# Optimization experiments

Hardware: AMD Instinct MI355X
Metric: run time of the kernel (lower is better)

## Reference

```python
import jax, jax.numpy as jnp
import numpy as np

B, L, K, D = 1, 4096, 24, 512


def setup_inputs() -> dict:
    key = jax.random.key(0)
    k1, k2, k3, k4 = jax.random.split(key, 4)
    u = jax.random.normal(k1, (B, L, D), dtype=jnp.float32)
    # spectral filter bank (learned parameter initialized from Hankel eigenvectors in the
    # original; random init is equivalent for a correctness baseline), scaled ~O(1/sqrt(L))
    filters = jax.random.normal(k2, (L, K), dtype=jnp.float32) * (1.0 / np.sqrt(L))
    M_phi_plus = jax.random.normal(k3, (K, D, D), dtype=jnp.float32) * (1.0 / np.sqrt(K * D))
    M_phi_minus = jax.random.normal(k4, (K, D, D), dtype=jnp.float32) * (1.0 / np.sqrt(K * D))
    return {"u": u, "filters": filters, "M_phi_plus": M_phi_plus, "M_phi_minus": M_phi_minus}


def _causal_conv(u, phi):
    # Causal linear convolution of every input channel with every spectral filter via FFT.
    # u: [B, L, D], phi: [L, K] -> [B, L, K, D]
    L_ = u.shape[1]
    n = 2 * L_  # zero-pad so circular FFT conv == linear causal conv
    Uf = jnp.fft.rfft(u, n=n, axis=1)                    # [B, F, D]
    Pf = jnp.fft.rfft(phi, n=n, axis=0)                  # [F, K]
    prod = Uf[:, :, None, :] * Pf[None, :, :, None]      # [B, F, K, D]
    return jnp.fft.irfft(prod, n=n, axis=1)[:, :L_]      # [B, L, K, D]


def reference(u, filters, M_phi_plus, M_phi_minus):
    L_ = u.shape[1]
    # sgn[t] = (-1)^t ; U_minus[b,l,k,d] = sum_s u[b,s,d] * phi[l-s,k] * (-1)^(l-s),
    # which equals convolving with the alternating-sign filter phi[t]*(-1)^t
    # (the original implements this as sgn-pre/post-multiplication around FlashFFTConv).
    sgn = jnp.where(jnp.arange(L_) % 2 == 0, 1.0, -1.0).astype(u.dtype)
    U_plus = _causal_conv(u, filters)                      # [B, L, K, D]
    U_minus = _causal_conv(u, filters * sgn[:, None])      # [B, L, K, D]
    y = (jnp.einsum('blkd,kdo->blo', U_plus, M_phi_plus)
         + jnp.einsum('blkd,kdo->blo', U_minus, M_phi_minus))
    return y
```

## Files before the change

### kernel.cpp

```cpp
#include <hip/hip_runtime.h>
#include <hip/hip_bf16.h>
#include <cstdint>
#include <cstddef>

using bf16 = __hip_bfloat16;

typedef __attribute__((ext_vector_type(4))) float f32x4;
typedef __attribute__((ext_vector_type(8))) short s16x8;

#define LSEQ 4096
#define DDIM 512
#define KFLT 24
#define NFFT 8192
#define FPAD 4224
#define MROWS 8448
#define FLIVE 8194

__device__ __forceinline__ void gld16(const bf16* g, bf16* l) {
  __builtin_amdgcn_global_load_lds((const __attribute__((address_space(1))) void*)g,
                                   (__attribute__((address_space(3))) void*)l, 16, 0, 0);
}

#define MEMFENCE asm volatile("" ::: "memory")
#define BAR() do { MEMFENCE; __builtin_amdgcn_s_barrier(); MEMFENCE; } while (0)

__device__ __forceinline__ float fsin_rev(float rev) {
  float s; asm("v_sin_f32 %0, %1" : "=v"(s) : "v"(rev)); return s;
}
__device__ __forceinline__ float fcos_rev(float rev) {
  float c; asm("v_cos_f32 %0, %1" : "=v"(c) : "v"(rev)); return c;
}

__device__ __forceinline__ void stage_half(const bf16* g, int ldk, bf16* ldsbase,
                                           int wave, int lane) {
  const int r8 = lane >> 3;
  const int sc = ((lane & 7) ^ r8) * 8;
  #pragma unroll
  for (int q = 0; q < 2; ++q) {
    const int c = wave * 2 + q;
    gld16(g + (size_t)(c * 8 + r8) * ldk + sc, ldsbase + c * 512);
  }
}

__device__ __forceinline__ s16x8 ldfrag(const bf16* buf, int row, int kk, int l4) {
  return *(const s16x8*)(buf + row * 64 + (((kk * 4 + l4) ^ (row & 7)) * 8));
}

__global__ __launch_bounds__(256) void transpose_cast(
    const float* __restrict__ in, bf16* __restrict__ out, int R, int C) {
  __shared__ float tile[32][33];
  const size_t bo = (size_t)blockIdx.z * R * C;
  const float* inb = in + bo;
  bf16* outb = out + bo;
  int c0 = blockIdx.x * 32, r0 = blockIdx.y * 32;
  int tx = threadIdx.x & 31, ty = threadIdx.x >> 5;
  #pragma unroll
  for (int i = 0; i < 32; i += 8)
    tile[ty + i][tx] = inb[(size_t)(r0 + ty + i) * C + (c0 + tx)];
  __syncthreads();
  #pragma unroll
  for (int i = 0; i < 32; i += 8)
    outb[(size_t)(c0 + ty + i) * R + (r0 + tx)] = __float2bfloat16(tile[tx][ty + i]);
}

__global__ __launch_bounds__(256) void tr_reduce5(
    const float* __restrict__ P0, const float* __restrict__ P14,
    bf16* __restrict__ out) {
  __shared__ float tile[32][33];
  int c0 = blockIdx.x * 32, r0 = blockIdx.y * 32;
  int tx = threadIdx.x & 31, ty = threadIdx.x >> 5;
  const size_t MN = (size_t)MROWS * DDIM;
  #pragma unroll
  for (int i = 0; i < 32; i += 8) {
    size_t idx = (size_t)(r0 + ty + i) * DDIM + (c0 + tx);
    tile[ty + i][tx] = P0[idx] + P14[idx] + P14[idx + MN] +
                       P14[idx + 2 * MN] + P14[idx + 3 * MN];
  }
  __syncthreads();
  #pragma unroll
  for (int i = 0; i < 32; i += 8)
    out[(size_t)(c0 + ty + i) * MROWS + (r0 + tx)] = __float2bfloat16(tile[tx][ty + i]);
}

__global__ __launch_bounds__(256) void reduce4(
    const float* __restrict__ P, float* __restrict__ y) {
  size_t i = ((size_t)blockIdx.x * 256 + threadIdx.x) * 4;
  const size_t MN = (size_t)LSEQ * DDIM;
  f32x4 a = *(const f32x4*)(P + i);
  f32x4 b = *(const f32x4*)(P + i + MN);
  f32x4 c = *(const f32x4*)(P + i + 2 * MN);
  f32x4 d = *(const f32x4*)(P + i + 3 * MN);
  *(f32x4*)(y + i) = a + b + c + d;
}

__global__ __launch_bounds__(256) void gen_w(bf16* __restrict__ W) {
  int r = blockIdx.y;
  int t0 = (blockIdx.x * 256 + threadIdx.x) * 8;
  bf16 o[8];
  if (r < FLIVE) {
    int f = r >> 1;
    bool odd = r & 1;
    #pragma unroll
    for (int i = 0; i < 8; ++i) {
      int m = (f * (t0 + i)) & (NFFT - 1);
      float rev = (float)m * (1.f / NFFT);
      float v = odd ? -fsin_rev(rev) : fcos_rev(rev);
      o[i] = __float2bfloat16(v);
    }
  } else {
    #pragma unroll
    for (int i = 0; i < 8; ++i) o[i] = __float2bfloat16(0.f);
  }
  *(s16x8*)(W + (size_t)r * LSEQ + t0) = *(const s16x8*)o;
}

__global__ __launch_bounds__(256) void gen_cinv(bf16* __restrict__ Cinv) {
  int l = blockIdx.y;
  int r0 = (blockIdx.x * 256 + threadIdx.x) * 8;
  if (r0 >= MROWS) return;
  bf16 o[8];
  #pragma unroll
  for (int p = 0; p < 4; ++p) {
    int rr = r0 + 2 * p;
    float v0 = 0.f, v1 = 0.f;
    if (rr < FLIVE) {
      int f = rr >> 1;
      int m = (f * l) & (NFFT - 1);
      float rev = (float)m * (1.f / NFFT);
      float wf = (f == 0 || f == NFFT / 2) ? 1.f : 2.f;
      float sc = wf * (1.f / NFFT);
      v0 = sc * fcos_rev(rev);
      v1 = -sc * fsin_rev(rev);
    }
    o[2 * p] = __float2bfloat16(v0);
    o[2 * p + 1] = __float2bfloat16(v1);
  }
  *(s16x8*)(Cinv + (size_t)l * MROWS + r0) = *(const s16x8*)o;
}

__global__ __launch_bounds__(256) void compute_pf(
    const float* __restrict__ phi, float* __restrict__ Pf) {
  int f = blockIdx.x;
  int tid = threadIdx.x;
  int lane = tid & 63, wave = tid >> 6;
  float pre[KFLT], pim[KFLT];
  #pragma unroll
  for (int k = 0; k < KFLT; ++k) { pre[k] = 0.f; pim[k] = 0.f; }
  for (int cch = 0; cch < LSEQ / 256; ++cch) {
    int t = cch * 256 + tid;
    int m = (f * t) & (NFFT - 1);
    float rev = (float)m * (1.f / NFFT);
    float s = fsin_rev(rev), c = fcos_rev(rev);
    const float4* pv = (const float4*)(phi + (size_t)t * KFLT);
    float4 v0 = pv[0], v1 = pv[1], v2 = pv[2], v3 = pv[3], v4 = pv[4], v5 = pv[5];
    float pr[KFLT] = {v0.x, v0.y, v0.z, v0.w, v1.x, v1.y, v1.z, v1.w,
                      v2.x, v2.y, v2.z, v2.w, v3.x, v3.y, v3.z, v3.w,
                      v4.x, v4.y, v4.z, v4.w, v5.x, v5.y, v5.z, v5.w};
    #pragma unroll
    for (int k = 0; k < KFLT; ++k) {
      pre[k] += pr[k] * c;
      pim[k] -= pr[k] * s;
    }
  }
  __shared__ float red[4][2 * KFLT];
  #pragma unroll
  for (int k = 0; k < KFLT; ++k) {
    float r = pre[k], i2 = pim[k];
    #pragma unroll
    for (int off = 32; off > 0; off >>= 1) {
      r += __shfl_down(r, off, 64);
      i2 += __shfl_down(i2, off, 64);
    }
    if (lane == 0) { red[wave][2 * k] = r; red[wave][2 * k + 1] = i2; }
  }
  __syncthreads();
  if (tid < 2 * KFLT)
    Pf[(size_t)f * (2 * KFLT) + tid] =
        red[0][tid] + red[1][tid] + red[2][tid] + red[3][tid];
}

__global__ __launch_bounds__(256) void build_pw(
    const float* __restrict__ Pf, float* __restrict__ Pw) {
  int idx = blockIdx.x * 256 + threadIdx.x;
  if (idx >= 48 * FPAD) return;
  int j = idx / FPAD, f = idx % FPAD;
  float re = 0.f, im = 0.f;
  if (f <= NFFT / 2) {
    if (j < KFLT) {
      re = Pf[(size_t)f * 48 + j * 2];
      im = Pf[(size_t)f * 48 + j * 2 + 1];
    } else {
      int k = j - KFLT, g = NFFT / 2 - f;
      re = Pf[(size_t)g * 48 + k * 2];
      im = -Pf[(size_t)g * 48 + k * 2 + 1];
    }
  }
  Pw[(size_t)idx * 2] = re;
  Pw[(size_t)idx * 2 + 1] = im;
}

template <int STORE>
__global__ __launch_bounds__(512, 2) void gemmD(
    const bf16* __restrict__ A, const bf16* __restrict__ Bt, int ldk,
    bf16* __restrict__ Obf, float* __restrict__ Of) {
  __shared__ bf16 sA[2 * 128 * 64];
  __shared__ bf16 sB[2 * 256 * 64];

  const int nwg = gridDim.x;
  const int lin = blockIdx.x;
  const int q8 = nwg >> 3, r8g = nwg & 7;
  const int xcd = lin & 7, pos = lin >> 3;
  const int wid = (xcd < r8g ? xcd * (q8 + 1) : r8g * (q8 + 1) + (xcd - r8g) * q8) + pos;

  int by, bx, kt0, nkt, ks;
  if constexpr (STORE == 0) { by = wid % 66; bx = wid / 66; kt0 = 0; nkt = 64; ks = 0; }
  else { int xy = wid & 63; ks = wid >> 6; by = xy >> 1; bx = xy & 1; kt0 = ks * 33; nkt = 33; }

  const int tid = threadIdx.x, lane = tid & 63, wave = tid >> 6;
  const int l15 = lane & 15, l4 = lane >> 4;
  const int wr = wave >> 2, wc = wave & 3;
  const int mtile = by * 128, ntile = bx * 256;
  const bf16* Ab = A + (size_t)mtile * ldk;
  const bf16* Bb = Bt + (size_t)ntile * ldk;

  f32x4 acc[4][4];
  #pragma unroll
  for (int m = 0; m < 4; ++m)
    #pragma unroll
    for (int n = 0; n < 4; ++n) acc[m][n] = f32x4{0.f, 0.f, 0.f, 0.f};

  stage_half(Ab + (size_t)kt0 * 64, ldk, sA, wave, lane);
  stage_half(Bb + (size_t)kt0 * 64, ldk, sB, wave, lane);
  stage_half(Bb + (size_t)128 * ldk + (size_t)kt0 * 64, ldk, sB + 128 * 64, wave, lane);
  asm volatile("s_waitcnt vmcnt(0)" ::: "memory");
  BAR();

  for (int t = 0; t < nkt; ++t) {
    const int par = t & 1, nb = par ^ 1;
    const bf16* bA = sA + par * (128 * 64);
    const bf16* bB = sB + par * (256 * 64);
    const bool more = (t + 1 < nkt);

    s16x8 afr[4][2], bfr[4][2];
    #pragma unroll
    for (int n = 0; n < 4; ++n)
      #pragma unroll
      for (int kk = 0; kk < 2; ++kk)
        bfr[n][kk] = ldfrag(bB, wc * 64 + n * 16 + l15, kk, l4);
    #pragma unroll
    for (int m = 0; m < 4; ++m)
      #pragma unroll
      for (int kk = 0; kk < 2; ++kk)
        afr[m][kk] = ldfrag(bA, wr * 64 + m * 16 + l15, kk, l4);

    if (more) {
      const size_t ko = (size_t)(kt0 + t + 1) * 64;
      stage_half(Ab + ko, ldk, sA + nb * (128 * 64), wave, lane);
      stage_half(Bb + ko, ldk, sB + nb * (256 * 64), wave, lane);
      stage_half(Bb + (size_t)128 * ldk + ko, ldk, sB + nb * (256 * 64) + 128 * 64,
                 wave, lane);
    }

    __builtin_amdgcn_s_setprio(1);
    #pragma unroll
    for (int m = 0; m < 4; ++m)
      #pragma unroll
      for (int n = 0; n < 4; ++n)
        #pragma unroll
        for (int kk = 0; kk < 2; ++kk)
          acc[m][n] = __builtin_amdgcn_mfma_f32_16x16x32_bf16(
              afr[m][kk], bfr[n][kk], acc[m][n], 0, 0, 0);
    __builtin_amdgcn_s_setprio(0);

    asm volatile("s_waitcnt vmcnt(0)" ::: "memory");
    BAR();
  }

  #pragma unroll
  for (int m = 0; m < 4; ++m)
    #pragma unroll
    for (int n = 0; n < 4; ++n)
      #pragma unroll
      for (int e = 0; e < 4; ++e) {
        int row = mtile + wr * 64 + m * 16 + l4 * 4 + e;
        int col = ntile + wc * 64 + n * 16 + l15;
        if constexpr (STORE == 0)
          Obf[(size_t)row * DDIM + col] = __float2bfloat16(acc[m][n][e]);
        else
          Of[(size_t)ks * LSEQ * DDIM + (size_t)row * DDIM + col] = acc[m][n][e];
      }
}

__global__ __launch_bounds__(512, 2) void gemmW(
    const bf16* __restrict__ Auf, const bf16* __restrict__ Mt,
    const float* __restrict__ Pw, float* __restrict__ P0, float* __restrict__ P14) {
  __shared__ bf16 sA[2 * 256 * 64];
  __shared__ bf16 sB[2 * 256 * 64];

  const int lin = blockIdx.x;
  const int wid = (lin & 7) * 32 + (lin >> 3);
  const int tid = threadIdx.x, lane = tid & 63, wave = tid >> 6;
  const int l15 = lane & 15, l4 = lane >> 4;
  const int wr = wave >> 2, wc = wave & 3;
  const int r8 = lane >> 3, c8 = lane & 7;
  const float sgn = (r8 & 1) ? 1.f : -1.f;

  const int g0 = wid * 99, g1 = g0 + 99;

  float* dst = (wid % 5 == 0) ? P0
             : P14 + (size_t)(wid % 5 - 1) * ((size_t)MROWS * DDIM);

  f32x4 acc[8][4];
  #pragma unroll
  for (int m = 0; m < 8; ++m)
    #pragma unroll
    for (int n = 0; n < 4; ++n) acc[m][n] = f32x4{0.f, 0.f, 0.f, 0.f};

  int4 adat[4];
  float2 wv[4];

  auto decode = [&](int g, int& mt, int& nt, int& j, int& kt, int& xy) {
    xy = g / 384; int rem = g - xy * 384; j = rem >> 3; kt = rem & 7;
    mt = (xy % 33) * 256; nt = (xy / 33) * 256;
  };
  auto issueA = [&](int mt, int j, int kt) {
    #pragma unroll
    for (int q = 0; q < 4; ++q) {
      int rl = (q >> 1) * 128 + (wave * 2 + (q & 1)) * 8 + r8;
      int rowg = mt + rl;
      adat[q] = *(const int4*)(Auf + (size_t)rowg * DDIM + kt * 64 + c8 * 8);
      wv[q] = *(const float2*)(Pw + ((size_t)j * FPAD + (rowg >> 1)) * 2);
    }
  };
  auto writeA = [&](bf16* dstbase) {
    #pragma unroll
    for (int q = 0; q < 4; ++q) {
      int rl = (q >> 1) * 128 + (wave * 2 + (q & 1)) * 8 + r8;
      int4 p;
      p.x = __shfl_xor(adat[q].x, 8, 64);
      p.y = __shfl_xor(adat[q].y, 8, 64);
      p.z = __shfl_xor(adat[q].z, 8, 64);
      p.w = __shfl_xor(adat[q].w, 8, 64);
      union { int4 i; unsigned short u[8]; } su, pu;
      su.i = adat[q]; pu.i = p;
      bf16 ob[8];
      #pragma unroll
      for (int e = 0; e < 8; ++e) {
        float fs = __uint_as_float((unsigned)su.u[e] << 16);
        float fp = __uint_as_float((unsigned)pu.u[e] << 16);
        ob[e] = __float2bfloat16(wv[q].x * fs + sgn * (wv[q].y * fp));
      }
      *(s16x8*)(dstbase + rl * 64 + ((c8 ^ r8) * 8)) = *(const s16x8*)ob;
    }
  };
  auto stageB = [&](int nt, int j, int kt, bf16* db) {
    const bf16* bb = Mt + (size_t)j * (DDIM * DDIM) + (size_t)nt * DDIM + kt * 64;
    stage_half(bb, DDIM, db, wave, lane);
    stage_half(bb + (size_t)128 * DDIM, DDIM, db + 128 * 64, wave, lane);
  };

  int mt, nt, j, kt, xy;
  decode(g0, mt, nt, j, kt, xy);
  issueA(mt, j, kt);
  stageB(nt, j, kt, sB);
  asm volatile("s_waitcnt vmcnt(4)" ::: "memory");
  writeA(sA);
  asm volatile("s_waitcnt vmcnt(0) lgkmcnt(0)" ::: "memory");
  BAR();

  int cxy = xy, cmt = mt, cnt_ = nt;

  for (int g = g0; g < g1; ++g) {
    const int par = (g - g0) & 1, nb = par ^ 1;
    const bf16* bA = sA + par * (256 * 64);
    const bf16* bB = sB + par * (256 * 64);
    const bool more = (g + 1 < g1);
    int nmt = 0, nnt = 0, nj = 0, nkt = 0, nxy = cxy;
    if (more) decode(g + 1, nmt, nnt, nj, nkt, nxy);

    s16x8 bfr[4][2], afr[4][2];
    #pragma unroll
    for (int n = 0; n < 4; ++n)
      #pragma unroll
      for (int kk = 0; kk < 2; ++kk)
        bfr[n][kk] = ldfrag(bB, wc * 64 + n * 16 + l15, kk, l4);
    #pragma unroll
    for (int m = 0; m < 4; ++m)
      #pragma unroll
      for (int kk = 0; kk < 2; ++kk)
        afr[m][kk] = ldfrag(bA, wr * 128 + m * 16 + l15, kk, l4);
    if (more) {
      issueA(nmt, nj, nkt);
      stageB(nnt, nj, nkt, sB + nb * (256 * 64));
    }
    __builtin_amdgcn_s_setprio(1);
    #pragma unroll
    for (int m = 0; m < 4; ++m)
      #pragma unroll
      for (int n = 0; n < 4; ++n)
        #pragma unroll
        for (int kk = 0; kk < 2; ++kk)
          acc[m][n] = __builtin_amdgcn_mfma_f32_16x16x32_bf16(
              afr[m][kk], bfr[n][kk], acc[m][n], 0, 0, 0);
    __builtin_amdgcn_s_setprio(0);

    #pragma unroll
    for (int m = 0; m < 4; ++m)
      #pragma unroll
      for (int kk = 0; kk < 2; ++kk)
        afr[m][kk] = ldfrag(bA, wr * 128 + 64 + m * 16 + l15, kk, l4);
    if (more) {
      asm volatile("s_waitcnt vmcnt(4)" ::: "memory");
      writeA(sA + nb * (256 * 64));
    }
    __builtin_amdgcn_s_setprio(1);
    #pragma unroll
    for (int m = 0; m < 4; ++m)
      #pragma unroll
      for (int n = 0; n < 4; ++n)
        #pragma unroll
        for (int kk = 0; kk < 2; ++kk)
          acc[4 + m][n] = __builtin_amdgcn_mfma_f32_16x16x32_bf16(
              afr[m][kk], bfr[n][kk], acc[4 + m][n], 0, 0, 0);
    __builtin_amdgcn_s_setprio(0);

    asm volatile("s_waitcnt vmcnt(0) lgkmcnt(0)" ::: "memory");
    BAR();

    if (!more || nxy != cxy) {
      #pragma unroll
      for (int m = 0; m < 8; ++m)
        #pragma unroll
        for (int n = 0; n < 4; ++n) {
          #pragma unroll
          for (int e = 0; e < 4; ++e) {
            int row = cmt + wr * 128 + (m & 3) * 16 + (m >> 2) * 64 + l4 * 4 + e;
            int col = cnt_ + wc * 64 + n * 16 + l15;
            dst[(size_t)row * DDIM + col] = acc[m][n][e];
          }
          acc[m][n] = f32x4{0.f, 0.f, 0.f, 0.f};
        }
    }
    cxy = nxy; cmt = nmt; cnt_ = nnt;
  }
}

#define WS_W     0ULL
#define WS_AUF   69206016ULL
#define WS_UT    77856768ULL
#define WS_MT    82051072ULL
#define WS_PF    107216896ULL
#define WS_PW    108003520ULL
#define WS_YSUM  109625536ULL
#define WS_YBT   126927040ULL
#define WS_TOTAL 135577792ULL

extern "C" void kernel_launch(void* const* d_in, const int* in_sizes, int n_in,
                              void* d_out, int out_size, void* d_ws, size_t ws_size,
                              hipStream_t stream) {
  const float* u   = (const float*)d_in[0];
  const float* phi = (const float*)d_in[1];
  const float* Mp  = (const float*)d_in[2];
  const float* Mm  = (const float*)d_in[3];
  float* y = (float*)d_out;

  if (ws_size < WS_TOTAL) return;

  char* ws = (char*)d_ws;
  bf16*  W    = (bf16*)(ws + WS_W);
  bf16*  Auf  = (bf16*)(ws + WS_AUF);
  bf16*  uT   = (bf16*)(ws + WS_UT);
  bf16*  Mt   = (bf16*)(ws + WS_MT);
  float* Pf   = (float*)(ws + WS_PF);
  float* Pw   = (float*)(ws + WS_PW);
  float* Ysum = (float*)(ws + WS_YSUM);
  bf16*  Ybt  = (bf16*)(ws + WS_YBT);
  float* P14  = (float*)(ws + WS_W);
  float* G3P  = (float*)(ws + WS_AUF);

  transpose_cast<<<dim3(16, 128, 1), 256, 0, stream>>>(u, uT, LSEQ, DDIM);
  transpose_cast<<<dim3(16, 16, 24), 256, 0, stream>>>(Mp, Mt, DDIM, DDIM);
  transpose_cast<<<dim3(16, 16, 24), 256, 0, stream>>>(Mm, Mt + (size_t)24 * DDIM * DDIM,
                                                       DDIM, DDIM);
  gen_w<<<dim3(2, MROWS), 256, 0, stream>>>(W);
  compute_pf<<<dim3(4097), 256, 0, stream>>>(phi, Pf);
  build_pw<<<dim3((48 * FPAD + 255) / 256), 256, 0, stream>>>(Pf, Pw);

  gemmD<0><<<132, 512, 0, stream>>>(W, uT, LSEQ, Auf, nullptr);

  hipMemsetAsync(Ysum, 0, (size_t)MROWS * DDIM * sizeof(float), stream);
  hipMemsetAsync(P14, 0, 4ULL * MROWS * DDIM * sizeof(float), stream);
  gemmW<<<256, 512, 0, stream>>>(Auf, Mt, Pw, Ysum, P14);

  tr_reduce5<<<dim3(16, 264), 256, 0, stream>>>(Ysum, P14, Ybt);
  gen_cinv<<<dim3(5, LSEQ), 256, 0, stream>>>(W);

  gemmD<1><<<256, 512, 0, stream>>>(W, Ybt, MROWS, nullptr, G3P);
  reduce4<<<dim3(LSEQ * DDIM / (256 * 4)), 256, 0, stream>>>(G3P, y);
}
```

Baseline: 583.0 us.

## Drop Nyquist bin from DFT GEMMs, handle it separately, and restructure GEMM work splits

Trims the padded frequency dimension from 8448 to 8192 rows by removing the Nyquist bin from the DFT-as-GEMM path and adding its contribution back through small dedicated kernels (nyq_u, vnyq_k) folded into the final reduction. The forward DFT GEMM becomes split-K across 256 workgroups with bf16 partials plus an add kernel. gemmW switches from a flattened work-list with dynamic tile flushes to a fixed per-workgroup (m-tile, n-tile, filter-group) assignment that writes its slot once, which removes the memsets. compute_pf does two frequencies per block. In exchange there are more small kernels, and the bf16 split-K partials lose some precision.

```diff
diff --git a/kernel.cpp b/kernel.cpp
--- a/kernel.cpp
+++ b/kernel.cpp
@@ -12,9 +12,7 @@
 #define DDIM 512
 #define KFLT 24
 #define NFFT 8192
-#define FPAD 4224
-#define MROWS 8448
-#define FLIVE 8194
+#define MR 8192
 
 __device__ __forceinline__ void gld16(const bf16* g, bf16* l) {
   __builtin_amdgcn_global_load_lds((const __attribute__((address_space(1))) void*)g,
@@ -63,53 +61,71 @@
     outb[(size_t)(c0 + ty + i) * R + (r0 + tx)] = __float2bfloat16(tile[tx][ty + i]);
 }
 
-__global__ __launch_bounds__(256) void tr_reduce5(
-    const float* __restrict__ P0, const float* __restrict__ P14,
-    bf16* __restrict__ out) {
+__global__ __launch_bounds__(256) void add2_cast(
+    const bf16* __restrict__ P, bf16* __restrict__ out) {
+  size_t i = ((size_t)blockIdx.x * 256 + threadIdx.x) * 8;
+  const size_t MN = (size_t)MR * DDIM;
+  s16x8 a = *(const s16x8*)(P + i);
+  s16x8 b = *(const s16x8*)(P + i + MN);
+  bf16 o[8];
+  #pragma unroll
+  for (int e = 0; e < 8; ++e) {
+    float fa = __uint_as_float((unsigned)(unsigned short)a[e] << 16);
+    float fb = __uint_as_float((unsigned)(unsigned short)b[e] << 16);
+    o[e] = __float2bfloat16(fa + fb);
+  }
+  *(s16x8*)(out + i) = *(const s16x8*)o;
+}
+
+__global__ __launch_bounds__(256) void tr_reduce4(
+    const float* __restrict__ S, bf16* __restrict__ out) {
   __shared__ float tile[32][33];
   int c0 = blockIdx.x * 32, r0 = blockIdx.y * 32;
   int tx = threadIdx.x & 31, ty = threadIdx.x >> 5;
-  const size_t MN = (size_t)MROWS * DDIM;
+  const int nt = c0 >> 8;
+  const int scl = (c0 & 255) + tx;
+  const size_t SB = (size_t)MR * 256;
   #pragma unroll
   for (int i = 0; i < 32; i += 8) {
-    size_t idx = (size_t)(r0 + ty + i) * DDIM + (c0 + tx);
-    tile[ty + i][tx] = P0[idx] + P14[idx] + P14[idx + MN] +
-                       P14[idx + 2 * MN] + P14[idx + 3 * MN];
+    size_t ro = (size_t)(r0 + ty + i) * 256 + scl;
+    tile[ty + i][tx] = S[(0 * 2 + nt) * SB + ro] + S[(1 * 2 + nt) * SB + ro] +
+                       S[(2 * 2 + nt) * SB + ro] + S[(3 * 2 + nt) * SB + ro];
   }
   __syncthreads();
   #pragma unroll
   for (int i = 0; i < 32; i += 8)
-    out[(size_t)(c0 + ty + i) * MROWS + (r0 + tx)] = __float2bfloat16(tile[tx][ty + i]);
-}
-
-__global__ __launch_bounds__(256) void reduce4(
-    const float* __restrict__ P, float* __restrict__ y) {
+    out[(size_t)(c0 + ty + i) * MR + (r0 + tx)] = __float2bfloat16(tile[tx][ty + i]);
+}
+
+__global__ __launch_bounds__(256) void reduce4y(
+    const float* __restrict__ P, const float* __restrict__ vnyq,
+    float* __restrict__ y) {
   size_t i = ((size_t)blockIdx.x * 256 + threadIdx.x) * 4;
   const size_t MN = (size_t)LSEQ * DDIM;
+  int l = (int)(i >> 9), o = (int)(i & 511);
   f32x4 a = *(const f32x4*)(P + i);
   f32x4 b = *(const f32x4*)(P + i + MN);
   f32x4 c = *(const f32x4*)(P + i + 2 * MN);
   f32x4 d = *(const f32x4*)(P + i + 3 * MN);
-  *(f32x4*)(y + i) = a + b + c + d;
+  f32x4 v = *(const f32x4*)(vnyq + o);
+  float sg = (l & 1) ? -(1.f / NFFT) : (1.f / NFFT);
+  f32x4 r = a + b + c + d;
+  r[0] += sg * v[0]; r[1] += sg * v[1]; r[2] += sg * v[2]; r[3] += sg * v[3];
+  *(f32x4*)(y + i) = r;
 }
 
 __global__ __launch_bounds__(256) void gen_w(bf16* __restrict__ W) {
   int r = blockIdx.y;
   int t0 = (blockIdx.x * 256 + threadIdx.x) * 8;
+  int f = r >> 1;
+  bool odd = r & 1;
   bf16 o[8];
-  if (r < FLIVE) {
-    int f = r >> 1;
-    bool odd = r & 1;
-    #pragma unroll
-    for (int i = 0; i < 8; ++i) {
-      int m = (f * (t0 + i)) & (NFFT - 1);
-      float rev = (float)m * (1.f / NFFT);
-      float v = odd ? -fsin_rev(rev) : fcos_rev(rev);
-      o[i] = __float2bfloat16(v);
-    }
-  } else {
-    #pragma unroll
-    for (int i = 0; i < 8; ++i) o[i] = __float2bfloat16(0.f);
+  #pragma unroll
+  for (int i = 0; i < 8; ++i) {
+    int m = (f * (t0 + i)) & (NFFT - 1);
+    float rev = (float)m * (1.f / NFFT);
+    float v = odd ? -fsin_rev(rev) : fcos_rev(rev);
+    o[i] = __float2bfloat16(v);
   }
   *(s16x8*)(W + (size_t)r * LSEQ + t0) = *(const s16x8*)o;
 }
@@ -117,86 +133,122 @@
 __global__ __launch_bounds__(256) void gen_cinv(bf16* __restrict__ Cinv) {
   int l = blockIdx.y;
   int r0 = (blockIdx.x * 256 + threadIdx.x) * 8;
-  if (r0 >= MROWS) return;
   bf16 o[8];
   #pragma unroll
   for (int p = 0; p < 4; ++p) {
-    int rr = r0 + 2 * p;
-    float v0 = 0.f, v1 = 0.f;
-    if (rr < FLIVE) {
-      int f = rr >> 1;
-      int m = (f * l) & (NFFT - 1);
-      float rev = (float)m * (1.f / NFFT);
-      float wf = (f == 0 || f == NFFT / 2) ? 1.f : 2.f;
-      float sc = wf * (1.f / NFFT);
-      v0 = sc * fcos_rev(rev);
-      v1 = -sc * fsin_rev(rev);
-    }
-    o[2 * p] = __float2bfloat16(v0);
-    o[2 * p + 1] = __float2bfloat16(v1);
-  }
-  *(s16x8*)(Cinv + (size_t)l * MROWS + r0) = *(const s16x8*)o;
+    int f = (r0 >> 1) + p;
+    int m = (f * l) & (NFFT - 1);
+    float rev = (float)m * (1.f / NFFT);
+    float sc = ((f == 0) ? 1.f : 2.f) * (1.f / NFFT);
+    o[2 * p] = __float2bfloat16(sc * fcos_rev(rev));
+    o[2 * p + 1] = __float2bfloat16(-sc * fsin_rev(rev));
+  }
+  *(s16x8*)(Cinv + (size_t)l * MR + r0) = *(const s16x8*)o;
 }
 
 __global__ __launch_bounds__(256) void compute_pf(
     const float* __restrict__ phi, float* __restrict__ Pf) {
-  int f = blockIdx.x;
+  int f0 = blockIdx.x * 2;
   int tid = threadIdx.x;
   int lane = tid & 63, wave = tid >> 6;
-  float pre[KFLT], pim[KFLT];
-  #pragma unroll
-  for (int k = 0; k < KFLT; ++k) { pre[k] = 0.f; pim[k] = 0.f; }
+  float pre[2][KFLT], pim[2][KFLT];
+  #pragma unroll
+  for (int ff = 0; ff < 2; ++ff)
+    #pragma unroll
+    for (int k = 0; k < KFLT; ++k) { pre[ff][k] = 0.f; pim[ff][k] = 0.f; }
   for (int cch = 0; cch < LSEQ / 256; ++cch) {
     int t = cch * 256 + tid;
-    int m = (f * t) & (NFFT - 1);
-    float rev = (float)m * (1.f / NFFT);
-    float s = fsin_rev(rev), c = fcos_rev(rev);
     const float4* pv = (const float4*)(phi + (size_t)t * KFLT);
     float4 v0 = pv[0], v1 = pv[1], v2 = pv[2], v3 = pv[3], v4 = pv[4], v5 = pv[5];
     float pr[KFLT] = {v0.x, v0.y, v0.z, v0.w, v1.x, v1.y, v1.z, v1.w,
                       v2.x, v2.y, v2.z, v2.w, v3.x, v3.y, v3.z, v3.w,
                       v4.x, v4.y, v4.z, v4.w, v5.x, v5.y, v5.z, v5.w};
     #pragma unroll
+    for (int ff = 0; ff < 2; ++ff) {
+      int m = ((f0 + ff) * t) & (NFFT - 1);
+      float rev = (float)m * (1.f / NFFT);
+      float s = fsin_rev(rev), c = fcos_rev(rev);
+      #pragma unroll
+      for (int k = 0; k < KFLT; ++k) {
+        pre[ff][k] += pr[k] * c;
+        pim[ff][k] -= pr[k] * s;
+      }
+    }
+  }
+  __shared__ float red[4][2][2 * KFLT];
+  #pragma unroll
+  for (int ff = 0; ff < 2; ++ff)
+    #pragma unroll
     for (int k = 0; k < KFLT; ++k) {
-      pre[k] += pr[k] * c;
-      pim[k] -= pr[k] * s;
-    }
-  }
-  __shared__ float red[4][2 * KFLT];
-  #pragma unroll
-  for (int k = 0; k < KFLT; ++k) {
-    float r = pre[k], i2 = pim[k];
-    #pragma unroll
-    for (int off = 32; off > 0; off >>= 1) {
-      r += __shfl_down(r, off, 64);
-      i2 += __shfl_down(i2, off, 64);
-    }
-    if (lane == 0) { red[wave][2 * k] = r; red[wave][2 * k + 1] = i2; }
-  }
+      float r = pre[ff][k], i2 = pim[ff][k];
+      #pragma unroll
+      for (int off = 32; off > 0; off >>= 1) {
+        r += __shfl_down(r, off, 64);
+        i2 += __shfl_down(i2, off, 64);
+      }
+      if (lane == 0) { red[wave][ff][2 * k] = r; red[wave][ff][2 * k + 1] = i2; }
+    }
   __syncthreads();
-  if (tid < 2 * KFLT)
-    Pf[(size_t)f * (2 * KFLT) + tid] =
-        red[0][tid] + red[1][tid] + red[2][tid] + red[3][tid];
+  if (tid < 96) {
+    int ff = tid / 48, q = tid % 48;
+    int f = f0 + ff;
+    if (f <= NFFT / 2)
+      Pf[(size_t)f * 48 + q] =
+          red[0][ff][q] + red[1][ff][q] + red[2][ff][q] + red[3][ff][q];
+  }
 }
 
 __global__ __launch_bounds__(256) void build_pw(
-    const float* __restrict__ Pf, float* __restrict__ Pw) {
+    const float* __restrict__ Pf, float* __restrict__ Pw, float* __restrict__ wnyq) {
   int idx = blockIdx.x * 256 + threadIdx.x;
-  if (idx >= 48 * FPAD) return;
-  int j = idx / FPAD, f = idx % FPAD;
-  float re = 0.f, im = 0.f;
-  if (f <= NFFT / 2) {
-    if (j < KFLT) {
-      re = Pf[(size_t)f * 48 + j * 2];
-      im = Pf[(size_t)f * 48 + j * 2 + 1];
-    } else {
-      int k = j - KFLT, g = NFFT / 2 - f;
-      re = Pf[(size_t)g * 48 + k * 2];
-      im = -Pf[(size_t)g * 48 + k * 2 + 1];
-    }
+  int j = idx >> 12, f = idx & 4095;
+  float re, im;
+  if (j < KFLT) {
+    re = Pf[(size_t)f * 48 + j * 2];
+    im = Pf[(size_t)f * 48 + j * 2 + 1];
+  } else {
+    int k = j - KFLT, g = NFFT / 2 - f;
+    re = Pf[(size_t)g * 48 + k * 2];
+    im = -Pf[(size_t)g * 48 + k * 2 + 1];
   }
   Pw[(size_t)idx * 2] = re;
   Pw[(size_t)idx * 2 + 1] = im;
+  if (idx < 48)
+    wnyq[idx] = (idx < KFLT) ? Pf[(size_t)(NFFT / 2) * 48 + idx * 2]
+                             : Pf[(idx - KFLT) * 2];
+}
+
+__global__ __launch_bounds__(256) void nyq_u(
+    const float* __restrict__ u, float* __restrict__ Unyq) {
+  int d = blockIdx.x * 256 + threadIdx.x;
+  float acc = 0.f;
+  for (int t = 0; t < LSEQ; t += 2)
+    acc += u[(size_t)t * DDIM + d] - u[(size_t)(t + 1) * DDIM + d];
+  Unyq[d] = acc;
+}
+
+__global__ __launch_bounds__(256) void vnyq_k(
+    const bf16* __restrict__ Mt, const float* __restrict__ Unyq,
+    const float* __restrict__ wnyq, float* __restrict__ vnyq) {
+  __shared__ float us[DDIM];
+  int j = blockIdx.x, tid = threadIdx.x;
+  us[tid] = Unyq[tid];
+  us[tid + 256] = Unyq[tid + 256];
+  __syncthreads();
+  float w = wnyq[j];
+  #pragma unroll
+  for (int h = 0; h < 2; ++h) {
+    int o = tid + h * 256;
+    const bf16* row = Mt + ((size_t)j * DDIM + o) * DDIM;
+    float acc = 0.f;
+    for (int d0 = 0; d0 < DDIM; d0 += 8) {
+      s16x8 v = *(const s16x8*)(row + d0);
+      #pragma unroll
+      for (int e = 0; e < 8; ++e)
+        acc += us[d0 + e] * __uint_as_float((unsigned)(unsigned short)v[e] << 16);
+    }
+    atomicAdd(&vnyq[o], w * acc);
+  }
 }
 
 template <int STORE>
@@ -206,20 +258,22 @@
   __shared__ bf16 sA[2 * 128 * 64];
   __shared__ bf16 sB[2 * 256 * 64];
 
-  const int nwg = gridDim.x;
   const int lin = blockIdx.x;
-  const int q8 = nwg >> 3, r8g = nwg & 7;
-  const int xcd = lin & 7, pos = lin >> 3;
-  const int wid = (xcd < r8g ? xcd * (q8 + 1) : r8g * (q8 + 1) + (xcd - r8g) * q8) + pos;
-
-  int by, bx, kt0, nkt, ks;
-  if constexpr (STORE == 0) { by = wid % 66; bx = wid / 66; kt0 = 0; nkt = 64; ks = 0; }
-  else { int xy = wid & 63; ks = wid >> 6; by = xy >> 1; bx = xy & 1; kt0 = ks * 33; nkt = 33; }
+  const int wid = (lin & 7) * 32 + (lin >> 3);
+
+  int mt, nt, kt0, nkt, ks;
+  if constexpr (STORE == 0) {
+    ks = wid >> 7; int rem = wid & 127; mt = rem >> 1; nt = rem & 1;
+    kt0 = ks * 32; nkt = 32;
+  } else {
+    ks = wid >> 6; int rem = wid & 63; mt = rem >> 1; nt = rem & 1;
+    kt0 = ks * 32; nkt = 32;
+  }
 
   const int tid = threadIdx.x, lane = tid & 63, wave = tid >> 6;
   const int l15 = lane & 15, l4 = lane >> 4;
   const int wr = wave >> 2, wc = wave & 3;
-  const int mtile = by * 128, ntile = bx * 256;
+  const int mtile = mt * 128, ntile = nt * 256;
   const bf16* Ab = A + (size_t)mtile * ldk;
   const bf16* Bb = Bt + (size_t)ntile * ldk;
 
@@ -285,7 +339,8 @@
         int row = mtile + wr * 64 + m * 16 + l4 * 4 + e;
         int col = ntile + wc * 64 + n * 16 + l15;
         if constexpr (STORE == 0)
-          Obf[(size_t)row * DDIM + col] = __float2bfloat16(acc[m][n][e]);
+          Obf[(size_t)ks * MR * DDIM + (size_t)row * DDIM + col] =
+              __float2bfloat16(acc[m][n][e]);
         else
           Of[(size_t)ks * LSEQ * DDIM + (size_t)row * DDIM + col] = acc[m][n][e];
       }
@@ -293,22 +348,23 @@
 
 __global__ __launch_bounds__(512, 2) void gemmW(
     const bf16* __restrict__ Auf, const bf16* __restrict__ Mt,
-    const float* __restrict__ Pw, float* __restrict__ P0, float* __restrict__ P14) {
+    const float* __restrict__ Pw, float* __restrict__ Slots) {
   __shared__ bf16 sA[2 * 256 * 64];
   __shared__ bf16 sB[2 * 256 * 64];
 
   const int lin = blockIdx.x;
   const int wid = (lin & 7) * 32 + (lin >> 3);
+  const int xcd = wid >> 5, pos = wid & 31;
+  const int nt = xcd & 1, jg = xcd >> 1;
+  const int mt = pos;
+
   const int tid = threadIdx.x, lane = tid & 63, wave = tid >> 6;
   const int l15 = lane & 15, l4 = lane >> 4;
   const int wr = wave >> 2, wc = wave & 3;
   const int r8 = lane >> 3, c8 = lane & 7;
   const float sgn = (r8 & 1) ? 1.f : -1.f;
 
-  const int g0 = wid * 99, g1 = g0 + 99;
-
-  float* dst = (wid % 5 == 0) ? P0
-             : P14 + (size_t)(wid % 5 - 1) * ((size_t)MROWS * DDIM);
+  float* dst = Slots + (size_t)(jg * 2 + nt) * ((size_t)MR * 256);
 
   f32x4 acc[8][4];
   #pragma unroll
@@ -319,17 +375,13 @@
   int4 adat[4];
   float2 wv[4];
 
-  auto decode = [&](int g, int& mt, int& nt, int& j, int& kt, int& xy) {
-    xy = g / 384; int rem = g - xy * 384; j = rem >> 3; kt = rem & 7;
-    mt = (xy % 33) * 256; nt = (xy / 33) * 256;
-  };
-  auto issueA = [&](int mt, int j, int kt) {
+  auto issueA = [&](int j, int kt) {
     #pragma unroll
     for (int q = 0; q < 4; ++q) {
       int rl = (q >> 1) * 128 + (wave * 2 + (q & 1)) * 8 + r8;
-      int rowg = mt + rl;
+      int rowg = mt * 256 + rl;
       adat[q] = *(const int4*)(Auf + (size_t)rowg * DDIM + kt * 64 + c8 * 8);
-      wv[q] = *(const float2*)(Pw + ((size_t)j * FPAD + (rowg >> 1)) * 2);
+      wv[q] = *(const float2*)(Pw + ((size_t)j * 4096 + (rowg >> 1)) * 2);
     }
   };
   auto writeA = [&](bf16* dstbase) {
@@ -353,30 +405,25 @@
       *(s16x8*)(dstbase + rl * 64 + ((c8 ^ r8) * 8)) = *(const s16x8*)ob;
     }
   };
-  auto stageB = [&](int nt, int j, int kt, bf16* db) {
-    const bf16* bb = Mt + (size_t)j * (DDIM * DDIM) + (size_t)nt * DDIM + kt * 64;
+  auto stageB = [&](int j, int kt, bf16* db) {
+    const bf16* bb = Mt + (size_t)j * (DDIM * DDIM) + (size_t)(nt * 256) * DDIM + kt * 64;
     stage_half(bb, DDIM, db, wave, lane);
     stage_half(bb + (size_t)128 * DDIM, DDIM, db + 128 * 64, wave, lane);
   };
 
-  int mt, nt, j, kt, xy;
-  decode(g0, mt, nt, j, kt, xy);
-  issueA(mt, j, kt);
-  stageB(nt, j, kt, sB);
+  issueA(jg * 12, 0);
+  stageB(jg * 12, 0, sB);
   asm volatile("s_waitcnt vmcnt(4)" ::: "memory");
   writeA(sA);
   asm volatile("s_waitcnt vmcnt(0) lgkmcnt(0)" ::: "memory");
   BAR();
 
-  int cxy = xy, cmt = mt, cnt_ = nt;
-
-  for (int g = g0; g < g1; ++g) {
-    const int par = (g - g0) & 1, nb = par ^ 1;
+  for (int s = 0; s < 96; ++s) {
+    const int par = s & 1, nb = par ^ 1;
     const bf16* bA = sA + par * (256 * 64);
     const bf16* bB = sB + par * (256 * 64);
-    const bool more = (g + 1 < g1);
-    int nmt = 0, nnt = 0, nj = 0, nkt = 0, nxy = cxy;
-    if (more) decode(g + 1, nmt, nnt, nj, nkt, nxy);
+    const bool more = (s + 1 < 96);
+    const int njj = jg * 12 + ((s + 1) >> 3), nkt = (s + 1) & 7;
 
     s16x8 bfr[4][2], afr[4][2];
     #pragma unroll
@@ -390,8 +437,8 @@
       for (int kk = 0; kk < 2; ++kk)
         afr[m][kk] = ldfrag(bA, wr * 128 + m * 16 + l15, kk, l4);
     if (more) {
-      issueA(nmt, nj, nkt);
-      stageB(nnt, nj, nkt, sB + nb * (256 * 64));
+      issueA(njj, nkt);
+      stageB(njj, nkt, sB + nb * (256 * 64));
     }
     __builtin_amdgcn_s_setprio(1);
     #pragma unroll
@@ -426,34 +473,32 @@
 
     asm volatile("s_waitcnt vmcnt(0) lgkmcnt(0)" ::: "memory");
     BAR();
-
-    if (!more || nxy != cxy) {
-      #pragma unroll
-      for (int m = 0; m < 8; ++m)
-        #pragma unroll
-        for (int n = 0; n < 4; ++n) {
-          #pragma unroll
-          for (int e = 0; e < 4; ++e) {
-            int row = cmt + wr * 128 + (m & 3) * 16 + (m >> 2) * 64 + l4 * 4 + e;
-            int col = cnt_ + wc * 64 + n * 16 + l15;
-            dst[(size_t)row * DDIM + col] = acc[m][n][e];
-          }
-          acc[m][n] = f32x4{0.f, 0.f, 0.f, 0.f};
-        }
-    }
-    cxy = nxy; cmt = nmt; cnt_ = nnt;
-  }
+  }
+
+  #pragma unroll
+  for (int m = 0; m < 8; ++m)
+    #pragma unroll
+    for (int n = 0; n < 4; ++n)
+      #pragma unroll
+      for (int e = 0; e < 4; ++e) {
+        int row = mt * 256 + wr * 128 + (m & 3) * 16 + (m >> 2) * 64 + l4 * 4 + e;
+        int col = wc * 64 + n * 16 + l15;
+        dst[(size_t)row * 256 + col] = acc[m][n][e];
+      }
 }
 
 #define WS_W     0ULL
-#define WS_AUF   69206016ULL
-#define WS_UT    77856768ULL
-#define WS_MT    82051072ULL
-#define WS_PF    107216896ULL
-#define WS_PW    108003520ULL
-#define WS_YSUM  109625536ULL
-#define WS_YBT   126927040ULL
-#define WS_TOTAL 135577792ULL
+#define WS_AUF   67108864ULL
+#define WS_UT    75497472ULL
+#define WS_MT    79691776ULL
+#define WS_PF    104857600ULL
+#define WS_PW    105644288ULL
+#define WS_WNYQ  107217152ULL
+#define WS_UNYQ  107217408ULL
+#define WS_VNYQ  107219456ULL
+#define WS_YBT   107221504ULL
+#define WS_G1P   115610112ULL
+#define WS_TOTAL 132387328ULL
 
 extern "C" void kernel_launch(void* const* d_in, const int* in_sizes, int n_in,
                               void* d_out, int out_size, void* d_ws, size_t ws_size,
@@ -468,33 +513,38 @@
 
   char* ws = (char*)d_ws;
   bf16*  W    = (bf16*)(ws + WS_W);
+  float* Slots= (float*)(ws + WS_W);
   bf16*  Auf  = (bf16*)(ws + WS_AUF);
   bf16*  uT   = (bf16*)(ws + WS_UT);
   bf16*  Mt   = (bf16*)(ws + WS_MT);
   float* Pf   = (float*)(ws + WS_PF);
   float* Pw   = (float*)(ws + WS_PW);
-  float* Ysum = (float*)(ws + WS_YSUM);
+  float* wny  = (float*)(ws + WS_WNYQ);
+  float* Uny  = (float*)(ws + WS_UNYQ);
+  float* vny  = (float*)(ws + WS_VNYQ);
   bf16*  Ybt  = (bf16*)(ws + WS_YBT);
-  float* P14  = (float*)(ws + WS_W);
+  bf16*  G1P  = (bf16*)(ws + WS_G1P);
   float* G3P  = (float*)(ws + WS_AUF);
 
   transpose_cast<<<dim3(16, 128, 1), 256, 0, stream>>>(u, uT, LSEQ, DDIM);
   transpose_cast<<<dim3(16, 16, 24), 256, 0, stream>>>(Mp, Mt, DDIM, DDIM);
   transpose_cast<<<dim3(16, 16, 24), 256, 0, stream>>>(Mm, Mt + (size_t)24 * DDIM * DDIM,
                                                        DDIM, DDIM);
-  gen_w<<<dim3(2, MROWS), 256, 0, stream>>>(W);
-  compute_pf<<<dim3(4097), 256, 0, stream>>>(phi, Pf);
-  build_pw<<<dim3((48 * FPAD + 255) / 256), 256, 0, stream>>>(Pf, Pw);
-
-  gemmD<0><<<132, 512, 0, stream>>>(W, uT, LSEQ, Auf, nullptr);
-
-  hipMemsetAsync(Ysum, 0, (size_t)MROWS * DDIM * sizeof(float), stream);
-  hipMemsetAsync(P14, 0, 4ULL * MROWS * DDIM * sizeof(float), stream);
-  gemmW<<<256, 512, 0, stream>>>(Auf, Mt, Pw, Ysum, P14);
-
-  tr_reduce5<<<dim3(16, 264), 256, 0, stream>>>(Ysum, P14, Ybt);
-  gen_cinv<<<dim3(5, LSEQ), 256, 0, stream>>>(W);
-
-  gemmD<1><<<256, 512, 0, stream>>>(W, Ybt, MROWS, nullptr, G3P);
-  reduce4<<<dim3(LSEQ * DDIM / (256 * 4)), 256, 0, stream>>>(G3P, y);
-}
+  gen_w<<<dim3(2, MR), 256, 0, stream>>>(W);
+  compute_pf<<<dim3(2049), 256, 0, stream>>>(phi, Pf);
+  build_pw<<<dim3(48 * 4096 / 256), 256, 0, stream>>>(Pf, Pw, wny);
+  nyq_u<<<dim3(2), 256, 0, stream>>>(u, Uny);
+
+  gemmD<0><<<256, 512, 0, stream>>>(W, uT, LSEQ, G1P, nullptr);
+  add2_cast<<<dim3(MR * DDIM / 2048), 256, 0, stream>>>(G1P, Auf);
+
+  gemmW<<<256, 512, 0, stream>>>(Auf, Mt, Pw, Slots);
+
+  tr_reduce4<<<dim3(16, 256), 256, 0, stream>>>(Slots, Ybt);
+  hipMemsetAsync(vny, 0, DDIM * sizeof(float), stream);
+  vnyq_k<<<dim3(48), 256, 0, stream>>>(Mt, Uny, wny, vny);
+
+  gen_cinv<<<dim3(4, LSEQ), 256, 0, stream>>>(W);
+  gemmD<1><<<256, 512, 0, stream>>>(W, Ybt, MR, nullptr, G3P);
+  reduce4y<<<dim3(LSEQ * DDIM / 1024), 256, 0, stream>>>(G3P, vny, y);
+}
```

Result: slower. 675.8 us (+15.9%).
